# Performance work log

Hardware: AMD Instinct MI355X
Metric: run time of the kernel (lower is better)

Reference implementation:

```python
import jax, jax.numpy as jnp
import numpy as np

GRID = 128
N0 = 262144
CHANNELS = [16, 32, 64, 128, 256]
EPS = 1e-5
OFFS2 = [(dx, dy, dz) for dx in (0, 1) for dy in (0, 1) for dz in (0, 1)]
OFFS3 = [(dx, dy, dz) for dx in (-1, 0, 1) for dy in (-1, 0, 1) for dz in (-1, 0, 1)]


def _keys(c, size):
    return (c[:, 0].astype(np.int64) * size + c[:, 1]) * size + c[:, 2]


def _rulebook(in_coords, out_coords, offsets, size_in, stride):
    # explicit-GEMM rulebook: for each kernel offset, (input_idx, output_idx) pairs,
    # padded to n_out with a validity mask so shapes are static.
    ik = _keys(in_coords, size_in)
    order = np.argsort(ik)
    sk = ik[order]
    K, P = len(offsets), out_coords.shape[0]
    I = np.zeros((K, P), np.int32)
    O = np.zeros((K, P), np.int32)
    M = np.zeros((K, P), bool)
    for k, off in enumerate(offsets):
        nbr = out_coords * stride + np.asarray(off)
        valid = np.all((nbr >= 0) & (nbr < size_in), axis=1)
        nk = _keys(np.clip(nbr, 0, size_in - 1), size_in)
        pos = np.minimum(np.searchsorted(sk, nk), len(sk) - 1)
        found = valid & (sk[pos] == nk)
        cnt = int(found.sum())
        I[k, :cnt] = order[pos[found]]
        O[k, :cnt] = np.nonzero(found)[0]
        M[k, :cnt] = True
    return I, O, M


def setup_inputs() -> dict:
    rng = np.random.RandomState(0)
    flat = rng.choice(GRID ** 3, size=N0, replace=False)
    coords = np.stack([flat // (GRID * GRID), (flat // GRID) % GRID, flat % GRID], 1).astype(np.int64)
    key = jax.random.key(0)
    ctr = [0]
    def nrm(shape, scale=1.0):
        ctr[0] += 1
        return scale * jax.random.normal(jax.random.fold_in(key, ctr[0]), shape, jnp.float32)
    inp = {"x": nrm((N0, CHANNELS[0]))}
    size = GRID
    for l in range(4):
        cin, cout = CHANNELS[l], CHANNELS[l + 1]
        out_coords = np.unique(coords // 2, axis=0)
        dI, dO, dM = _rulebook(coords, out_coords, OFFS2, size, 2)       # stride-2, k=2 down conv
        bI, bO, bM = _rulebook(out_coords, out_coords, OFFS3, size // 2, 1)  # stride-1, k=3 block conv
        inp[f"dW{l}"] = nrm((8, cin, cout), (8 * cin) ** -0.5)
        inp[f"dI{l}"] = jnp.asarray(dI); inp[f"dO{l}"] = jnp.asarray(dO); inp[f"dM{l}"] = jnp.asarray(dM)
        inp[f"dG{l}"] = 1.0 + nrm((cout,), 0.1)
        inp[f"dB{l}"] = nrm((cout,), 0.1)
        inp[f"dN{l}"] = int(out_coords.shape[0])
        inp[f"bW{l}"] = nrm((27, cout, cout), (27 * cout) ** -0.5)
        inp[f"bC{l}"] = nrm((cout,), 0.01)
        inp[f"bI{l}"] = jnp.asarray(bI); inp[f"bO{l}"] = jnp.asarray(bO); inp[f"bM{l}"] = jnp.asarray(bM)
        inp[f"bG{l}"] = 1.0 + nrm((cout,), 0.1)
        inp[f"bH{l}"] = nrm((cout,), 0.1)
        coords = out_coords
        size //= 2
    return inp


def _conv(f, W, I, O, M, n_out, bias=None):
    # gather -> GEMM -> scatter-add, one pass per kernel offset (fixed small K)
    out = jnp.zeros((n_out, W.shape[-1]), f.dtype)
    for k in range(W.shape[0]):
        g = jnp.where(M[k][:, None], f[I[k]], 0.0)
        out = out.at[O[k]].add(g @ W[k])
    return out if bias is None else out + bias


def _bn_relu(f, g, b):
    # training-mode BatchNorm over active voxels, fused with ReLU
    m = f.mean(0)
    v = jnp.mean((f - m) ** 2, 0)
    return jax.nn.relu((f - m) * (g * jax.lax.rsqrt(v + EPS)) + b)


def _forward(x, levels):
    outs = [x]
    for (dW, dI, dO, dM, dG, dB, dN, bW, bC, bI, bO, bM, bG, bH) in levels:
        x = _bn_relu(_conv(x, dW, dI, dO, dM, dN), dG, dB)        # down block (bias=False)
        x = _bn_relu(_conv(x, bW, bI, bO, bM, dN, bC), bG, bH)    # ConvBlock
        outs.append(x)
    return tuple(outs)


def reference(x, dW0, dI0, dO0, dM0, dG0, dB0, dN0, bW0, bC0, bI0, bO0, bM0, bG0, bH0,
              dW1, dI1, dO1, dM1, dG1, dB1, dN1, bW1, bC1, bI1, bO1, bM1, bG1, bH1,
              dW2, dI2, dO2, dM2, dG2, dB2, dN2, bW2, bC2, bI2, bO2, bM2, bG2, bH2,
              dW3, dI3, dO3, dM3, dG3, dB3, dN3, bW3, bC3, bI3, bO3, bM3, bG3, bH3):
    levels = [
        (dW0, dI0, dO0, dM0, dG0, dB0, dN0, bW0, bC0, bI0, bO0, bM0, bG0, bH0),
        (dW1, dI1, dO1, dM1, dG1, dB1, dN1, bW1, bC1, bI1, bO1, bM1, bG1, bH1),
        (dW2, dI2, dO2, dM2, dG2, dB2, dN2, bW2, bC2, bI2, bO2, bM2, bG2, bH2),
        (dW3, dI3, dO3, dM3, dG3, dB3, dN3, bW3, bC3, bI3, bO3, bM3, bG3, bH3),
    ]
    return _forward(x, levels)
```

## Files before the change

kernel.cpp:

```cpp
#include <hip/hip_runtime.h>
#include <hip/hip_bf16.h>
#include <stdint.h>
#include <stddef.h>

typedef __hip_bfloat16 bf16;
typedef __attribute__((ext_vector_type(8))) short bf8_t;
typedef __attribute__((ext_vector_type(4))) float f4_t;
static const int CH[5] = {16, 32, 64, 128, 256};

__device__ __forceinline__ float b2f(unsigned short u) {
    return __uint_as_float(((unsigned int)u) << 16);
}
__device__ __forceinline__ unsigned short f2bu(float f) {
    union { bf16 h; unsigned short u; } cv;
    cv.h = __float2bfloat16(f);
    return cv.u;
}
__device__ __forceinline__ void fma4(float4& a, float s, const float4& w) {
    a.x = fmaf(s, w.x, a.x);
    a.y = fmaf(s, w.y, a.y);
    a.z = fmaf(s, w.z, a.z);
    a.w = fmaf(s, w.w, a.w);
}
struct us4 { unsigned short a, b, c, d; };

__global__ void k_sentinel(float* __restrict__ out, float v) {
    if (threadIdx.x == 0) out[0] = v;
}

__global__ void SparseConvEncoder_20633022890309_kernel(
        const unsigned char* __restrict__ bM0, int* __restrict__ flag) {
    if (threadIdx.x == 0) {
        flag[0] = 1;
        flag[1] = 0;
        flag[2] = (bM0[0] == 1 && bM0[1] == 0 && bM0[2] == 0 && bM0[3] == 0 && bM0[4] == 1) ? 1 : 0;
    }
}

__global__ void __launch_bounds__(256) k_copy(const float* __restrict__ x,
                                              float* __restrict__ y, long n) {
    long i = (long)blockIdx.x * 256 + threadIdx.x;
    if (i < n) y[i] = x[i];
}

__global__ void __launch_bounds__(256) k_copytob(const float* __restrict__ x,
                                                 float* __restrict__ y,
                                                 unsigned short* __restrict__ yb, long n) {
    long i = (long)blockIdx.x * 256 + threadIdx.x;
    if (i < n) {
        float v = x[i];
        y[i] = v;
        yb[i] = f2bu(v);
    }
}

__global__ void __launch_bounds__(256) k_wt2(const float* __restrict__ dW,
                                             unsigned short* __restrict__ dWt, int dcin,
                                             const float* __restrict__ bW,
                                             unsigned short* __restrict__ bWt, int bcin,
                                             int cout, long dtot, long btot) {
    long i = (long)blockIdx.x * 256 + threadIdx.x;
    if (i < dtot) {
        long cc = (long)dcin * cout;
        int k = (int)(i / cc);
        int rem = (int)(i % cc);
        int co = rem / dcin, ci = rem % dcin;
        dWt[i] = f2bu(dW[((long)k * dcin + ci) * cout + co]);
    } else if (i < dtot + btot) {
        long j = i - dtot;
        long cc = (long)bcin * cout;
        int k = (int)(j / cc);
        int rem = (int)(j % cc);
        int co = rem / bcin, ci = rem % bcin;
        bWt[j] = f2bu(bW[((long)k * bcin + ci) * cout + co]);
    }
}

__global__ void __launch_bounds__(256) k_scatter(const int* __restrict__ I,
                                                 const int* __restrict__ O,
                                                 const void* __restrict__ M,
                                                 const int* __restrict__ flag,
                                                 int* __restrict__ R, int P, int k0, int cnt) {
    int i = blockIdx.x * 256 + threadIdx.x;
    if (i >= cnt) return;
    long gi = (long)k0 * P + i;
    int m = flag[2] ? ((const int*)M)[gi] : (int)((const unsigned char*)M)[gi];
    if (!m) return;
    R[(long)(i / P) * P + O[gi]] = I[gi];
}

__global__ void __launch_bounds__(256) k_init(float* __restrict__ out,
                                              const float* __restrict__ bias,
                                              long total, int maskC) {
    long i = (long)blockIdx.x * 256 + threadIdx.x;
    if (i < total) out[i] = bias ? bias[i & maskC] : 0.f;
}

template <int CIN, int TN, int MODE, int KT>
__global__ void __launch_bounds__(256) k_mconv(const unsigned short* __restrict__ Xb,
                                               const unsigned short* __restrict__ Wt,
                                               const float* __restrict__ bias,
                                               const int* __restrict__ R,
                                               float* __restrict__ out,
                                               int n, int cout, int kcnt, int gs) {
    const int lane = threadIdx.x & 63;
    const int wave = threadIdx.x >> 6;
    const int rt = blockIdx.x * 4 + wave;
    const int row_tiles = (n + 15) >> 4;
    if (rt >= row_tiles) return;
    const int m = lane & 15, q = lane >> 4;
    const int o = rt * 16 + m;
    const int co0 = blockIdx.y * (16 * TN);
    const bf8_t zero = {};

    f4_t acc[TN];
#pragma unroll
    for (int t = 0; t < TN; ++t) {
        if (MODE == 0) {
            float bv = bias ? bias[co0 + t * 16 + m] : 0.f;
            acc[t][0] = bv; acc[t][1] = bv; acc[t][2] = bv; acc[t][3] = bv;
        } else if (MODE == 1) {
#pragma unroll
            for (int g = 0; g < 4; ++g) {
                int row = rt * 16 + q * 4 + g;
                acc[t][g] = (row < n) ? out[(long)row * cout + co0 + t * 16 + m] : 0.f;
            }
        } else {
            acc[t][0] = 0.f; acc[t][1] = 0.f; acc[t][2] = 0.f; acc[t][3] = 0.f;
        }
    }

    bool touched = (MODE != 2);

    if constexpr (KT > 0) {
        int r[KT];
#pragma unroll
        for (int kk = 0; kk < KT; ++kk)
            r[kk] = (o < n) ? R[(long)kk * n + o] : -1;

        if constexpr (CIN == 16) {
#pragma unroll
            for (int p = 0; p < KT / 2; ++p) {
                int rsel = (q < 2) ? r[2 * p] : r[2 * p + 1];
                long ax = (long)((rsel >= 0) ? rsel : 0) * CIN + (q & 1) * 8;
                bf8_t av = *(const bf8_t*)(Xb + ax);
                bf8_t a = (rsel >= 0) ? av : zero;
                int ksel = 2 * p + (q >> 1);
#pragma unroll
                for (int t = 0; t < TN; ++t) {
                    int co = co0 + t * 16 + m;
                    long bx = ((long)ksel * cout + co) * CIN + (q & 1) * 8;
                    bf8_t b = *(const bf8_t*)(Wt + bx);
                    acc[t] = __builtin_amdgcn_mfma_f32_16x16x32_bf16(a, b, acc[t], 0, 0, 0);
                }
            }
        } else {
#pragma unroll
            for (int kk = 0; kk < KT; ++kk) {
#pragma unroll
                for (int cb = 0; cb < CIN; cb += 32) {
                    long ax = (long)((r[kk] >= 0) ? r[kk] : 0) * CIN + cb + q * 8;
                    bf8_t av = *(const bf8_t*)(Xb + ax);
                    bf8_t a = (r[kk] >= 0) ? av : zero;
#pragma unroll
                    for (int t = 0; t < TN; ++t) {
                        int co = co0 + t * 16 + m;
                        long bx = ((long)kk * cout + co) * CIN + cb + q * 8;
                        bf8_t b = *(const bf8_t*)(Wt + bx);
                        acc[t] = __builtin_amdgcn_mfma_f32_16x16x32_bf16(a, b, acc[t], 0, 0, 0);
                    }
                }
            }
        }
    } else {
        int ks = 0, ke = kcnt;
        if (MODE == 2) {
            ks = blockIdx.z * gs;
            ke = ks + gs;
            if (ke > kcnt) ke = kcnt;
        }
        for (int kb = ks; kb < ke; kb += 4) {
            int r4[4];
#pragma unroll
            for (int j = 0; j < 4; ++j) {
                int kk = kb + j;
                r4[j] = (kk < ke && o < n) ? R[(long)kk * n + o] : -1;
            }
            if (MODE == 2) {
                unsigned long long bl =
                    __ballot((r4[0] >= 0) | (r4[1] >= 0) | (r4[2] >= 0) | (r4[3] >= 0));
                if (bl == 0ULL) continue;
                touched = true;
            }
#pragma unroll
            for (int j = 0; j < 4; ++j) {
                int kk = kb + j;
                if (kk >= ke) break;
                int r = r4[j];
#pragma unroll
                for (int cb = 0; cb < CIN; cb += 32) {
                    const bool kval = !(CIN == 16 && q >= 2);
                    const int kbase = kval ? (cb + q * 8) : 0;
                    long ax = (long)((r >= 0) ? r : 0) * CIN + kbase;
                    bf8_t av = *(const bf8_t*)(Xb + ax);
                    bf8_t a = (r >= 0 && kval) ? av : zero;
#pragma unroll
                    for (int t = 0; t < TN; ++t) {
                        int co = co0 + t * 16 + m;
                        long bx = ((long)kk * cout + co) * CIN + kbase;
                        bf8_t bv = *(const bf8_t*)(Wt + bx);
                        bf8_t b = kval ? bv : zero;
                        acc[t] = __builtin_amdgcn_mfma_f32_16x16x32_bf16(a, b, acc[t], 0, 0, 0);
                    }
                }
            }
        }
    }

    if (MODE == 2 && !touched) return;
#pragma unroll
    for (int t = 0; t < TN; ++t) {
#pragma unroll
        for (int g = 0; g < 4; ++g) {
            int row = rt * 16 + q * 4 + g;
            if (row >= n) continue;
            float* p = out + (long)row * cout + co0 + t * 16 + m;
            if (MODE == 2) atomicAdd(p, acc[t][g]);
            else *p = acc[t][g];
        }
    }
}

static void mconv_dispatch(int cin, int tn, int mode, int kt, dim3 grd,
                           const unsigned short* Xb, const unsigned short* Wt,
                           const float* bias, const int* R, float* out,
                           int n, int cout, int kcnt, int gs, hipStream_t stream) {
#define MF_(CC, TT, KK)                                                            \
    if (cin == CC && tn == TT && mode == 0 && kt == KK) {                          \
        k_mconv<CC, TT, 0, KK><<<grd, 256, 0, stream>>>(Xb, Wt, bias, R, out, n,   \
                                                        cout, kcnt, gs);           \
        return;                                                                    \
    }
    MF_(16, 2, 8) MF_(32, 4, 8) MF_(32, 2, 27) MF_(64, 4, 27)
#undef MF_
#define M3_(CC, TT, MM)                                                            \
    if (cin == CC && tn == TT && mode == MM) {                                     \
        k_mconv<CC, TT, MM, 0><<<grd, 256, 0, stream>>>(Xb, Wt, bias, R, out, n,   \
                                                        cout, kcnt, gs);           \
        return;                                                                    \
    }
#define M2_(CC) M3_(CC, 2, 0) M3_(CC, 2, 1) M3_(CC, 2, 2) \
                M3_(CC, 4, 0) M3_(CC, 4, 1) M3_(CC, 4, 2)
    M2_(16) M2_(32) M2_(64) M2_(128) M2_(256)
#undef M2_
#undef M3_
}

static void run_mconv(const unsigned short* Xb, const unsigned short* Wt,
                      const float* bias, const int* I, const int* O, const void* M,
                      const int* flag, int* R, float* out, int n, int cin, int cout,
                      int K, int G, hipStream_t stream) {
    int rt = (n + 15) / 16;
    int bx = (rt + 3) / 4;
    int tn = (cout >= 64) ? 4 : 2;
    int gy = cout / (16 * tn);
    long bxy = (long)bx * gy;
    int kg = 1;
    if (bxy < 512 && G >= K) {
        kg = (int)((1024 + bxy - 1) / bxy);
        if (kg > K) kg = K;
    }
    int gs = (K + kg - 1) / kg;
    kg = (K + gs - 1) / gs;

    if (kg > 1) {
        int cnt = K * n;
        hipMemsetAsync(R, 0xFF, (size_t)cnt * 4, stream);
        k_scatter<<<(cnt + 255) / 256, 256, 0, stream>>>(I, O, M, flag, R, n, 0, cnt);
        long tot = (long)n * cout;
        k_init<<<(int)((tot + 255) / 256), 256, 0, stream>>>(out, bias, tot, cout - 1);
        mconv_dispatch(cin, tn, 2, 0, dim3(bx, gy, kg), Xb, Wt, bias, R, out,
                       n, cout, K, gs, stream);
    } else {
        for (int k0 = 0; k0 < K; k0 += G) {
            int g = (K - k0 < G) ? (K - k0) : G;
            int cnt = g * n;
            hipMemsetAsync(R, 0xFF, (size_t)cnt * 4, stream);
            k_scatter<<<(cnt + 255) / 256, 256, 0, stream>>>(I, O, M, flag, R, n, k0, cnt);
            int kt = (k0 == 0 && g == K) ? K : 0;
            mconv_dispatch(cin, tn, (k0 == 0) ? 0 : 1, kt, dim3(bx, gy, 1), Xb,
                           Wt + (size_t)k0 * cout * cin, bias, R, out,
                           n, cout, g, g, stream);
        }
    }
}

template <int CIN, int ROWS, int XBF, int MODE>
__global__ void __launch_bounds__(256) k_conv_t(const void* __restrict__ X,
                                                const float* __restrict__ W,
                                                const float* __restrict__ bias,
                                                const int* __restrict__ R,
                                                float* __restrict__ out,
                                                int n, int cout,
                                                int wk0, int kcnt, int gs) {
    const int c4 = threadIdx.x;
    const int by = blockDim.y;
    const int base = blockIdx.x * by * ROWS;
    const float* Xf = (const float*)X;
    const unsigned short* Xb = (const unsigned short*)X;

    int o[ROWS];
    float4 acc[ROWS];
    bool touched[ROWS];
#pragma unroll
    for (int j = 0; j < ROWS; ++j) {
        o[j] = base + j * by + threadIdx.y;
        touched[j] = false;
        acc[j] = make_float4(0.f, 0.f, 0.f, 0.f);
        if (o[j] < n) {
            if (MODE == 0) {
                if (bias) acc[j] = *(const float4*)(bias + c4 * 4);
            } else if (MODE == 1) {
                acc[j] = *(const float4*)(out + (long)o[j] * cout + c4 * 4);
            }
        }
    }
    int ks = 0, ke = kcnt;
    if (MODE == 2) {
        ks = blockIdx.y * gs;
        ke = ks + gs;
        if (ke > kcnt) ke = kcnt;
    }
    for (int kk = ks; kk < ke; ++kk) {
        int r[ROWS];
        bool any = false;
#pragma unroll
        for (int j = 0; j < ROWS; ++j) {
            r[j] = (o[j] < n) ? R[(long)kk * n + o[j]] : -1;
            any = any || (r[j] >= 0);
            touched[j] = touched[j] || (r[j] >= 0);
        }
        if (!any) continue;
        const float* wk = W + ((long)(wk0 + kk) * CIN) * cout + c4 * 4;
#pragma unroll
        for (int ci = 0; ci < CIN; ci += 4) {
            float4 w0 = *(const float4*)(wk + (long)(ci + 0) * cout);
            float4 w1 = *(const float4*)(wk + (long)(ci + 1) * cout);
            float4 w2 = *(const float4*)(wk + (long)(ci + 2) * cout);
            float4 w3 = *(const float4*)(wk + (long)(ci + 3) * cout);
#pragma unroll
            for (int j = 0; j < ROWS; ++j) {
                if (r[j] < 0) continue;
                float x0, x1, x2, x3;
                if (XBF) {
                    us4 u = *(const us4*)(Xb + (long)r[j] * CIN + ci);
                    x0 = b2f(u.a); x1 = b2f(u.b); x2 = b2f(u.c); x3 = b2f(u.d);
                } else {
                    float4 xv = *(const float4*)(Xf + (long)r[j] * CIN + ci);
                    x0 = xv.x; x1 = xv.y; x2 = xv.z; x3 = xv.w;
                }
                fma4(acc[j], x0, w0);
                fma4(acc[j], x1, w1);
                fma4(acc[j], x2, w2);
                fma4(acc[j], x3, w3);
            }
        }
    }
#pragma unroll
    for (int j = 0; j < ROWS; ++j) {
        if (o[j] >= n) continue;
        if (MODE == 2) {
            if (!touched[j]) continue;
            float* p = out + (long)o[j] * cout + c4 * 4;
            atomicAdd(p + 0, acc[j].x);
            atomicAdd(p + 1, acc[j].y);
            atomicAdd(p + 2, acc[j].z);
            atomicAdd(p + 3, acc[j].w);
        } else {
            *(float4*)(out + (long)o[j] * cout + c4 * 4) = acc[j];
        }
    }
}

static void conv_dispatch(int cin, int rows, int xbf, int mode, dim3 grd, dim3 blk,
                          const void* X, const float* W, const float* bias,
                          const int* R, float* out, int n, int cout,
                          int wk0, int kcnt, int gs, hipStream_t stream) {
#define C3_(CC, RR, XB, MM)                                                        \
    if (cin == CC && rows == RR && xbf == XB && mode == MM) {                      \
        k_conv_t<CC, RR, XB, MM><<<grd, blk, 0, stream>>>(X, W, bias, R, out, n,   \
                                                          cout, wk0, kcnt, gs);    \
        return;                                                                    \
    }
#define C2_(CC, RR) C3_(CC, RR, 0, 0) C3_(CC, RR, 0, 1) C3_(CC, RR, 0, 2) \
                    C3_(CC, RR, 1, 0) C3_(CC, RR, 1, 1) C3_(CC, RR, 1, 2)
#define C1_(CC) C2_(CC, 1) C2_(CC, 2) C2_(CC, 4)
    C1_(16) C1_(32) C1_(64) C1_(128) C1_(256)
#undef C1_
#undef C2_
#undef C3_
}

static void run_conv(const void* X, int xbf, const float* W, const float* bias,
                     const int* I, const int* O, const void* M, const int* flag,
                     int* R, float* out, int n, int cin, int cout, int K,
                     int G, hipStream_t stream) {
    int bx = cout / 4, by = 256 / bx;
    int g4 = (n + by * 4 - 1) / (by * 4);
    int g2 = (n + by * 2 - 1) / (by * 2);
    int rows;
    if (g4 >= 1024) rows = 4;
    else if (g2 >= 1024) rows = 2;
    else rows = 1;
    int gridn = (n + by * rows - 1) / (by * rows);
    int kg = 1;
    if (gridn < 768 && G >= K) {
        kg = (2048 + gridn - 1) / gridn;
        if (kg > K) kg = K;
    }
    int gs = (K + kg - 1) / kg;
    kg = (K + gs - 1) / gs;
    dim3 blk(bx, by);
    if (kg > 1) {
        int cnt = K * n;
        hipMemsetAsync(R, 0xFF, (size_t)cnt * 4, stream);
        k_scatter<<<(cnt + 255) / 256, 256, 0, stream>>>(I, O, M, flag, R, n, 0, cnt);
        long tot = (long)n * cout;
        k_init<<<(int)((tot + 255) / 256), 256, 0, stream>>>(out, bias, tot, cout - 1);
        conv_dispatch(cin, rows, xbf, 2, dim3(gridn, kg), blk, X, W, bias, R, out,
                      n, cout, 0, K, gs, stream);
    } else {
        for (int k0 = 0; k0 < K; k0 += G) {
            int g = (K - k0 < G) ? (K - k0) : G;
            int cnt = g * n;
            hipMemsetAsync(R, 0xFF, (size_t)cnt * 4, stream);
            k_scatter<<<(cnt + 255) / 256, 256, 0, stream>>>(I, O, M, flag, R, n, k0, cnt);
            conv_dispatch(cin, rows, xbf, (k0 == 0) ? 0 : 1, dim3(gridn, 1), blk,
                          X, W, bias, R, out, n, cout, k0, g, g, stream);
        }
    }
}

__global__ void __launch_bounds__(256) k_stats(const float* __restrict__ X,
                                               float* __restrict__ sums, int n, int C) {
    int c = threadIdx.x, ty = threadIdx.y, ny = blockDim.y;
    float s1 = 0.f, s2 = 0.f;
    for (int o = blockIdx.x * ny + ty; o < n; o += gridDim.x * ny) {
        float v = X[(long)o * C + c];
        s1 += v;
        s2 += v * v;
    }
    __shared__ float sm[512];
    sm[ty * C + c] = s1;
    sm[256 + ty * C + c] = s2;
    __syncthreads();
    if (ty == 0) {
        for (int t = 1; t < ny; ++t) {
            s1 += sm[t * C + c];
            s2 += sm[256 + t * C + c];
        }
        atomicAdd(&sums[c], s1);
        atomicAdd(&sums[C + c], s2);
    }
}

__global__ void __launch_bounds__(256) k_apply(const float* __restrict__ X,
                                               const float* __restrict__ sums,
                                               const float* __restrict__ g,
                                               const float* __restrict__ b,
                                               void* __restrict__ Y, int ybf,
                                               unsigned short* __restrict__ Y2,
                                               long total, int maskC, int C, float inv_n) {
    long i = (long)blockIdx.x * 256 + threadIdx.x;
    if (i >= total) return;
    int c = (int)(i & (long)maskC);
    float mean = sums[c] * inv_n;
    float var = fmaf(-mean, mean, sums[C + c] * inv_n);
    float sc = g[c] * rsqrtf(var + 1e-5f);
    float sh = fmaf(-mean, sc, b[c]);
    float v = fmaf(X[i], sc, sh);
    v = v > 0.f ? v : 0.f;
    if (ybf) ((unsigned short*)Y)[i] = f2bu(v);
    else     ((float*)Y)[i] = v;
    if (Y2) Y2[i] = f2bu(v);
}

static void run_bn(const float* src, int n, int C, const float* g, const float* b,
                   void* dst, int dst_bf16, unsigned short* dst2,
                   float* sums, hipStream_t stream) {
    hipMemsetAsync(sums, 0, 2 * C * sizeof(float), stream);
    dim3 sblk(C, 256 / C);
    int sgrd = (n + (int)sblk.y - 1) / (int)sblk.y;
    if (sgrd > 1024) sgrd = 1024;
    k_stats<<<sgrd, sblk, 0, stream>>>(src, sums, n, C);
    long tot = (long)n * C;
    k_apply<<<(int)((tot + 255) / 256), 256, 0, stream>>>(src, sums, g, b, dst, dst_bf16,
                                                          dst2, tot, C - 1, C,
                                                          1.0f / (float)n);
}

extern "C" void kernel_launch(void* const* d_in, const int* in_sizes, int n_in,
                              void* d_out, int out_size, void* d_ws, size_t ws_size,
                              hipStream_t stream) {
    float* out = (float*)d_out;

    int stride = 0;
    if (n_in == 57) stride = 14;
    else if (n_in == 53) stride = 13;
    if (!stride) {
        k_sentinel<<<1, 64, 0, stream>>>(out, 10240.f + (float)n_in);
        return;
    }
    static const int o14[13] = {0, 1, 2, 3, 4, 5, 7, 8, 9, 10, 11, 12, 13};
    static const int o13[13] = {0, 1, 2, 3, 4, 5, 6, 7, 8, 9, 10, 11, 12};
    const int* om = (stride == 14) ? o14 : o13;

    long n0 = (long)in_sizes[0];
    int P[4];
    bool ok = (n0 % 16 == 0);
    long total = n0;
    for (int l = 0; l < 4 && ok; ++l) {
        int base = 1 + stride * l;
        int sdI = in_sizes[base + om[1]], sdO = in_sizes[base + om[2]], sdM = in_sizes[base + om[3]];
        int sbI = in_sizes[base + om[8]], sbO = in_sizes[base + om[9]], sbM = in_sizes[base + om[10]];
        if (sdI <= 0 || sdI % 8 != 0 || sdO != sdI || sdM != sdI) { ok = false; break; }
        int p = sdI / 8;
        if (sbI != 27 * p || sbO != sbI || sbM != sbI) { ok = false; break; }
        if (in_sizes[base + om[0]] != 8 * CH[l] * CH[l + 1]) { ok = false; break; }
        if (in_sizes[base + om[6]] != 27 * CH[l + 1] * CH[l + 1]) { ok = false; break; }
        P[l] = p;
        total += (long)p * CH[l + 1];
    }
    if (!ok) {
        k_sentinel<<<1, 64, 0, stream>>>(out, 49152.f);
        return;
    }
    if (total != (long)out_size) {
        k_sentinel<<<1, 64, 0, stream>>>(out, 53248.f);
        return;
    }

    auto al = [](size_t x) { return (x + 255) / 256 * 256; };
    size_t maxBuf = 0, maxP = 0, maxXb = 0;
    long rowsIn[4] = {n0 / 16, P[0], P[1], P[2]};
    for (int l = 0; l < 4; ++l) {
        size_t b = (size_t)P[l] * CH[l + 1];
        if (b > maxBuf) maxBuf = b;
        if ((size_t)P[l] > maxP) maxP = (size_t)P[l];
        size_t xi = (size_t)rowsIn[l] * CH[l];
        if (xi > maxXb) maxXb = xi;
    }
    const size_t fixed = 4096;
    size_t rmin = al(maxP * 4);
    size_t dwt_sz = al((size_t)8 * 128 * 256 * 2);
    size_t bwt_sz = al((size_t)27 * 256 * 256 * 2);
    size_t mf_need = dwt_sz + bwt_sz + al(maxXb * 2) + al(maxBuf * 2) + fixed + rmin;

    if (ws_size >= mf_need) {
        char* wsp = (char*)d_ws;
        unsigned short* dWt = (unsigned short*)wsp; wsp += dwt_sz;
        unsigned short* bWt = (unsigned short*)wsp; wsp += bwt_sz;
        unsigned short* xb = (unsigned short*)wsp;  wsp += al(maxXb * 2);
        unsigned short* bufB = (unsigned short*)wsp; wsp += al(maxBuf * 2);
        float* sums = (float*)wsp; wsp += 1024;
        int* flag = (int*)wsp;     wsp += 2048;
        int* R = (int*)wsp;
        size_t Rbytes = ws_size - (size_t)(wsp - (char*)d_ws);

        SparseConvEncoder_20633022890309_kernel<<<1, 64, 0, stream>>>(
            (const unsigned char*)d_in[1 + om[10]], flag);
        k_copytob<<<(int)((n0 + 255) / 256), 256, 0, stream>>>((const float*)d_in[0],
                                                               out, xb, n0);

        long coff = n0;
        for (int l = 0; l < 4; ++l) {
            int base = 1 + stride * l;
            const float* dW = (const float*)d_in[base + om[0]];
            const int* dI = (const int*)d_in[base + om[1]];
            const int* dO = (const int*)d_in[base + om[2]];
            const void* dM = d_in[base + om[3]];
            const float* dG = (const float*)d_in[base + om[4]];
            const float* dB = (const float*)d_in[base + om[5]];
            const float* bW = (const float*)d_in[base + om[6]];
            const float* bC = (const float*)d_in[base + om[7]];
            const int* bI = (const int*)d_in[base + om[8]];
            const int* bO = (const int*)d_in[base + om[9]];
            const void* bM = d_in[base + om[10]];
            const float* bG = (const float*)d_in[base + om[11]];
            const float* bH = (const float*)d_in[base + om[12]];
            int n = P[l], cin = CH[l], cout = CH[l + 1];

            int G = (int)(Rbytes / ((size_t)n * 4));
            if (G > 27) G = 27;
            if (G < 1) G = 1;

            float* chunkp = out + coff;

            long dwtot = (long)8 * cin * cout;
            long bwtot = (long)27 * cout * cout;
            k_wt2<<<(int)((dwtot + bwtot + 255) / 256), 256, 0, stream>>>(
                dW, dWt, cin, bW, bWt, cout, cout, dwtot, bwtot);

            run_mconv(xb, dWt, nullptr, dI, dO, dM, flag, R, chunkp,
                      n, cin, cout, 8, (G > 8) ? 8 : G, stream);
            run_bn(chunkp, n, cout, dG, dB, bufB, 1, nullptr, sums, stream);

            run_mconv(bufB, bWt, bC, bI, bO, bM, flag, R, chunkp,
                      n, cout, cout, 27, G, stream);
            run_bn(chunkp, n, cout, bG, bH, chunkp, 0,
                   (l < 3) ? xb : nullptr, sums, stream);

            coff += (long)n * cout;
        }
        return;
    }

    int bufB_bf16;
    size_t bufBytes;
    if (ws_size >= fixed + al(maxBuf * 4) + rmin) { bufB_bf16 = 0; bufBytes = al(maxBuf * 4); }
    else if (ws_size >= fixed + al(maxBuf * 2) + rmin) { bufB_bf16 = 1; bufBytes = al(maxBuf * 2); }
    else {
        k_sentinel<<<1, 64, 0, stream>>>(out, 16384.f + (float)(ws_size >> 20));
        return;
    }
    size_t Rbytes = ws_size - fixed - bufBytes;
    char* wsp = (char*)d_ws;
    void* bufB = (void*)wsp;   wsp += bufBytes;
    float* sums = (float*)wsp; wsp += 1024;
    int* flag = (int*)wsp;     wsp += 2048;
    int* R = (int*)wsp;

    SparseConvEncoder_20633022890309_kernel<<<1, 64, 0, stream>>>(
        (const unsigned char*)d_in[1 + om[10]], flag);
    k_copy<<<(int)((n0 + 255) / 256), 256, 0, stream>>>((const float*)d_in[0], out, n0);

    long coff = n0;
    const void* cur_in = d_in[0];
    int cur_xbf = 0;
    for (int l = 0; l < 4; ++l) {
        int base = 1 + stride * l;
        const float* dW = (const float*)d_in[base + om[0]];
        const int* dI = (const int*)d_in[base + om[1]];
        const int* dO = (const int*)d_in[base + om[2]];
        const void* dM = d_in[base + om[3]];
        const float* dG = (const float*)d_in[base + om[4]];
        const float* dB = (const float*)d_in[base + om[5]];
        const float* bW = (const float*)d_in[base + om[6]];
        const float* bC = (const float*)d_in[base + om[7]];
        const int* bI = (const int*)d_in[base + om[8]];
        const int* bO = (const int*)d_in[base + om[9]];
        const void* bM = d_in[base + om[10]];
        const float* bG = (const float*)d_in[base + om[11]];
        const float* bH = (const float*)d_in[base + om[12]];
        int n = P[l], cin = CH[l], cout = CH[l + 1];

        int G = (int)(Rbytes / ((size_t)n * 4));
        if (G > 27) G = 27;
        if (G < 1) G = 1;

        float* chunkp = out + coff;
        run_conv(cur_in, cur_xbf, dW, nullptr, dI, dO, dM, flag, R, chunkp,
                 n, cin, cout, 8, (G > 8) ? 8 : G, stream);
        run_bn(chunkp, n, cout, dG, dB, bufB, bufB_bf16, nullptr, sums, stream);
        run_conv(bufB, bufB_bf16, bW, bC, bI, bO, bM, flag, R, chunkp,
                 n, cout, cout, 27, G, stream);
        run_bn(chunkp, n, cout, bG, bH, chunkp, 0, nullptr, sums, stream);

        cur_in = (const void*)chunkp;
        cur_xbf = 0;
        coff += (long)n * cout;
    }
}
```

Before: 830.3 us.

## Batch gathered activation loads ahead of MFMA chains and shrink tiles for small grids

Restructures the sparse-conv MFMA kernel so that gathered A-fragment loads for a group of kernel offsets are issued up front into register arrays, before the MFMA loops consume them. This exposes more memory-level parallelism for the irregular gathers. The register arrays raise register pressure and may reduce occupancy. It also adds more fixed-KT template instantiations and switches to TN=2 when the block grid is small, which creates more blocks at the cost of less reuse of loaded A fragments.

After: 834.2 us. Within noise of the previous version (+0.5%).

```diff
diff --git a/kernel.cpp b/kernel.cpp
--- a/kernel.cpp
+++ b/kernel.cpp
@@ -139,35 +139,54 @@
             r[kk] = (o < n) ? R[(long)kk * n + o] : -1;
 
         if constexpr (CIN == 16) {
+            bf8_t a[KT / 2];
 #pragma unroll
             for (int p = 0; p < KT / 2; ++p) {
                 int rsel = (q < 2) ? r[2 * p] : r[2 * p + 1];
                 long ax = (long)((rsel >= 0) ? rsel : 0) * CIN + (q & 1) * 8;
                 bf8_t av = *(const bf8_t*)(Xb + ax);
-                bf8_t a = (rsel >= 0) ? av : zero;
+                a[p] = (rsel >= 0) ? av : zero;
+            }
+#pragma unroll
+            for (int p = 0; p < KT / 2; ++p) {
                 int ksel = 2 * p + (q >> 1);
 #pragma unroll
                 for (int t = 0; t < TN; ++t) {
                     int co = co0 + t * 16 + m;
                     long bx = ((long)ksel * cout + co) * CIN + (q & 1) * 8;
                     bf8_t b = *(const bf8_t*)(Wt + bx);
-                    acc[t] = __builtin_amdgcn_mfma_f32_16x16x32_bf16(a, b, acc[t], 0, 0, 0);
+                    acc[t] = __builtin_amdgcn_mfma_f32_16x16x32_bf16(a[p], b, acc[t], 0, 0, 0);
                 }
             }
         } else {
-#pragma unroll
-            for (int kk = 0; kk < KT; ++kk) {
-#pragma unroll
-                for (int cb = 0; cb < CIN; cb += 32) {
-                    long ax = (long)((r[kk] >= 0) ? r[kk] : 0) * CIN + cb + q * 8;
-                    bf8_t av = *(const bf8_t*)(Xb + ax);
-                    bf8_t a = (r[kk] >= 0) ? av : zero;
-#pragma unroll
-                    for (int t = 0; t < TN; ++t) {
-                        int co = co0 + t * 16 + m;
-                        long bx = ((long)kk * cout + co) * CIN + cb + q * 8;
-                        bf8_t b = *(const bf8_t*)(Wt + bx);
-                        acc[t] = __builtin_amdgcn_mfma_f32_16x16x32_bf16(a, b, acc[t], 0, 0, 0);
+            constexpr int NC = CIN / 32;
+            constexpr int GB = (KT > 9) ? 9 : KT;
+#pragma unroll
+            for (int g0 = 0; g0 < KT; g0 += GB) {
+                bf8_t a[GB][NC];
+#pragma unroll
+                for (int j = 0; j < GB; ++j) {
+                    int kk = g0 + j;
+#pragma unroll
+                    for (int cb = 0; cb < NC; ++cb) {
+                        long ax = (long)((r[kk] >= 0) ? r[kk] : 0) * CIN + cb * 32 + q * 8;
+                        bf8_t av = *(const bf8_t*)(Xb + ax);
+                        a[j][cb] = (r[kk] >= 0) ? av : zero;
+                    }
+                }
+#pragma unroll
+                for (int j = 0; j < GB; ++j) {
+                    int kk = g0 + j;
+#pragma unroll
+                    for (int cb = 0; cb < NC; ++cb) {
+#pragma unroll
+                        for (int t = 0; t < TN; ++t) {
+                            int co = co0 + t * 16 + m;
+                            long bx = ((long)kk * cout + co) * CIN + cb * 32 + q * 8;
+                            bf8_t b = *(const bf8_t*)(Wt + bx);
+                            acc[t] = __builtin_amdgcn_mfma_f32_16x16x32_bf16(a[j][cb], b,
+                                                                             acc[t], 0, 0, 0);
+                        }
                     }
                 }
             }
@@ -179,38 +198,52 @@
             ke = ks + gs;
             if (ke > kcnt) ke = kcnt;
         }
-        for (int kb = ks; kb < ke; kb += 4) {
-            int r4[4];
-#pragma unroll
-            for (int j = 0; j < 4; ++j) {
+        constexpr int NC = (CIN >= 32) ? (CIN / 32) : 1;
+        constexpr int JB = (CIN >= 128) ? 2 : 4;
+        for (int kb = ks; kb < ke; kb += JB) {
+            int rj[JB];
+#pragma unroll
+            for (int j = 0; j < JB; ++j) {
                 int kk = kb + j;
-                r4[j] = (kk < ke && o < n) ? R[(long)kk * n + o] : -1;
+                rj[j] = (kk < ke && o < n) ? R[(long)kk * n + o] : -1;
             }
             if (MODE == 2) {
-                unsigned long long bl =
-                    __ballot((r4[0] >= 0) | (r4[1] >= 0) | (r4[2] >= 0) | (r4[3] >= 0));
-                if (bl == 0ULL) continue;
+                int any = 0;
+#pragma unroll
+                for (int j = 0; j < JB; ++j) any |= (rj[j] >= 0) ? 1 : 0;
+                if (__ballot(any) == 0ULL) continue;
                 touched = true;
             }
-#pragma unroll
-            for (int j = 0; j < 4; ++j) {
+            bf8_t a[JB][NC];
+#pragma unroll
+            for (int j = 0; j < JB; ++j) {
+                int kk = kb + j;
+                bool inb = (kk < ke) && (rj[j] >= 0);
+#pragma unroll
+                for (int cb = 0; cb < NC; ++cb) {
+                    const bool kval = !(CIN == 16 && q >= 2);
+                    const int kbase = (CIN == 16) ? (kval ? q * 8 : 0) : (cb * 32 + q * 8);
+                    long ax = (long)(inb ? rj[j] : 0) * CIN + kbase;
+                    bf8_t av = *(const bf8_t*)(Xb + ax);
+                    a[j][cb] = (inb && kval) ? av : zero;
+                }
+            }
+#pragma unroll
+            for (int j = 0; j < JB; ++j) {
                 int kk = kb + j;
                 if (kk >= ke) break;
-                int r = r4[j];
-#pragma unroll
-                for (int cb = 0; cb < CIN; cb += 32) {
+#pragma unroll
+                for (int cb = 0; cb < NC; ++cb) {
                     const bool kval = !(CIN == 16 && q >= 2);
-                    const int kbase = kval ? (cb + q * 8) : 0;
-                    long ax = (long)((r >= 0) ? r : 0) * CIN + kbase;
-                    bf8_t av = *(const bf8_t*)(Xb + ax);
-                    bf8_t a = (r >= 0 && kval) ? av : zero;
+                    const int kbase = (CIN == 16) ? (kval ? q * 8 : 0) : (cb * 32 + q * 8);
 #pragma unroll
                     for (int t = 0; t < TN; ++t) {
                         int co = co0 + t * 16 + m;
                         long bx = ((long)kk * cout + co) * CIN + kbase;
                         bf8_t bv = *(const bf8_t*)(Wt + bx);
                         bf8_t b = kval ? bv : zero;
-                        acc[t] = __builtin_amdgcn_mfma_f32_16x16x32_bf16(a, b, acc[t], 0, 0, 0);
+                        acc[t] = __builtin_amdgcn_mfma_f32_16x16x32_bf16(a[j][cb], b,
+                                                                         acc[t], 0, 0, 0);
                     }
                 }
             }
@@ -241,7 +274,8 @@
                                                         cout, kcnt, gs);           \
         return;                                                                    \
     }
-    MF_(16, 2, 8) MF_(32, 4, 8) MF_(32, 2, 27) MF_(64, 4, 27)
+    MF_(16, 2, 8) MF_(32, 2, 8) MF_(32, 4, 8) MF_(64, 2, 8) MF_(64, 4, 8)
+    MF_(32, 2, 27) MF_(64, 2, 27) MF_(64, 4, 27)
 #undef MF_
 #define M3_(CC, TT, MM)                                                            \
     if (cin == CC && tn == TT && mode == MM) {                                     \
@@ -264,6 +298,7 @@
     int bx = (rt + 3) / 4;
     int tn = (cout >= 64) ? 4 : 2;
     int gy = cout / (16 * tn);
+    if (tn == 4 && (long)bx * gy < 1024) { tn = 2; gy = cout / 32; }
     long bxy = (long)bx * gy;
     int kg = 1;
     if (bxy < 512 && G >= K) {
```
